# Kernel optimization log

Hardware: AMD Instinct MI355X
Metric: run time of the kernel (lower is better)

The kernel has to match this reference:

```python
import jax, jax.numpy as jnp
import numpy as np

K = 16  # hardcoded in the original forward
B, N, D = 4, 8192, 3


def _compute_normals_pca(x, k):
    """x: [B, N, 3] point cloud -> [B, N, 3] unit normals (smallest-eigvec of local covariance)."""
    sq = jnp.sum(x * x, axis=-1)  # [B, N]
    # squared pairwise distances [B, N, N]
    d2 = sq[:, :, None] + sq[:, None, :] - 2.0 * jnp.einsum('bnd,bmd->bnm', x, x)
    _, idx = jax.lax.top_k(-d2, k)  # k nearest (includes self), [B, N, k]
    # gather neighbor coordinates: [B, N, k, 3]
    nbrs = jax.vmap(lambda pts, i: pts[i])(x, idx)
    cen = nbrs - jnp.mean(nbrs, axis=2, keepdims=True)  # center per neighborhood
    cov = jnp.einsum('bnki,bnkj->bnij', cen, cen) / k   # [B, N, 3, 3]
    # eigh returns ascending eigenvalues; normal = eigvec of smallest eigenvalue (unit norm)
    evecs = jnp.linalg.eigh(cov)[1]
    return evecs[..., 0]  # [B, N, 3]


def setup_inputs() -> dict:
    key = jax.random.key(0)
    k1, k2 = jax.random.split(key)
    pred = jax.random.normal(k1, (B, N, D), dtype=jnp.float32)
    gt = jax.random.normal(k2, (B, N, D), dtype=jnp.float32)
    return {"pred": pred, "gt": gt}


def reference(pred, gt):
    n_pred = _compute_normals_pca(pred, K)
    n_gt = _compute_normals_pca(gt, K)
    return 1.0 - jnp.mean(jnp.sum(n_pred * n_gt, axis=-1))
```

## Files before the change

### kernel.cpp

```cpp
#include <hip/hip_runtime.h>
#include <math.h>


#define NPTS 8192
#define NB   4
#define QPW  4


__device__ __forceinline__ float slapy2f(float x, float y){
#pragma clang fp contract(off)
  float xa = fabsf(x), ya = fabsf(y);
  float w = fmaxf(xa, ya), z = fminf(xa, ya);
  if (z == 0.f) return w;
  float t = z / w;
  return w * sqrtf(1.f + t*t);
}

__device__ __forceinline__ void slartgf(float f, float g, float& c, float& s, float& r){
#pragma clang fp contract(off)
  const float safmin = 1.17549435e-38f;
  const float safmax = 8.50705917e37f;
  const float rtmin  = 1.08420217e-19f;
  const float rtmax  = 6.52318604e18f;
  if (g == 0.f){ c = 1.f; s = 0.f; r = f; }
  else if (f == 0.f){ c = 0.f; s = copysignf(1.f, g); r = fabsf(g); }
  else {
    float f1 = fabsf(f), g1 = fabsf(g);
    if (f1 > rtmin && f1 < rtmax && g1 > rtmin && g1 < rtmax){
      float d = sqrtf(f*f + g*g);
      c = f1 / d;
      r = copysignf(d, f);
      s = g / r;
    } else {
      float u = fminf(safmax, fmaxf(safmin, fmaxf(f1, g1)));
      float fs = f/u, gs = g/u;
      float d = sqrtf(fs*fs + gs*gs);
      c = fabsf(fs)/d;
      r = copysignf(d, f);
      r = r*u;
      s = g/r;
    }
  }
}

__device__ __forceinline__ void slaev2f(float a, float b, float cc,
                                        float& rt1, float& rt2, float& cs1, float& sn1){
#pragma clang fp contract(off)
  float sm  = a + cc;
  float df  = a - cc;
  float adf = fabsf(df);
  float tb  = b + b;
  float ab  = fabsf(tb);
  float acmx, acmn;
  if (fabsf(a) > fabsf(cc)){ acmx = a; acmn = cc; } else { acmx = cc; acmn = a; }
  float rt;
  if (adf > ab){ float t = ab/adf; rt = adf*sqrtf(1.f + t*t); }
  else if (adf < ab){ float t = adf/ab; rt = ab*sqrtf(1.f + t*t); }
  else rt = ab*sqrtf(2.f);
  int sgn1;
  if (sm < 0.f){ rt1 = 0.5f*(sm - rt); sgn1 = -1; rt2 = (acmx/rt1)*acmn - (b/rt1)*b; }
  else if (sm > 0.f){ rt1 = 0.5f*(sm + rt); sgn1 = 1; rt2 = (acmx/rt1)*acmn - (b/rt1)*b; }
  else { rt1 = 0.5f*rt; rt2 = -0.5f*rt; sgn1 = 1; }
  int sgn2; float cs;
  if (df >= 0.f){ cs = df + rt; sgn2 = 1; } else { cs = df - rt; sgn2 = -1; }
  float acs = fabsf(cs);
  if (acs > ab){ float ct = -tb/cs; sn1 = 1.f/sqrtf(1.f + ct*ct); cs1 = ct*sn1; }
  else {
    if (ab == 0.f){ cs1 = 1.f; sn1 = 0.f; }
    else { float tn = -cs/tb; cs1 = 1.f/sqrtf(1.f + tn*tn); sn1 = tn*cs1; }
  }
  if (sgn1 == sgn2){ float tn = cs1; cs1 = -sn1; sn1 = tn; }
}

__device__ __forceinline__ void rot2(float z[3][3], int ja, float c, float s){
#pragma clang fp contract(off)
  #pragma unroll
  for (int i = 0; i < 3; ++i){
    float t1 = z[i][ja+1];
    float t0 = z[i][ja];
    z[i][ja+1] = c*t1 - s*t0;
    z[i][ja]   = s*t1 + c*t0;
  }
}

__device__ __noinline__ void ssteqr3(float* d, float* e, float z[3][3]){
#pragma clang fp contract(off)
  const float eps    = 5.96046448e-08f;
  const float eps2   = 3.55271368e-15f;
  const float safmin = 1.17549435e-38f;
  const float ssfmax = 3.07445735e+18f;
  const float ssfmin = 3.05175781e-05f;
  const int n = 3;
  float cw[2], sw[2];
  int nmaxit, jtot, l1, l, lsv, lend, lendsv, m, iscale, i, j, ii, k;
  float anorm, p, g, r, c, s, f, b, rt1, rt2, tst, mul;

  for (i = 0; i < 3; ++i) for (j = 0; j < 3; ++j) z[i][j] = (i == j) ? 1.f : 0.f;
  nmaxit = n*30; jtot = 0; l1 = 1; m = 0; iscale = 0; anorm = 0.f;
  lsv = 1; lendsv = 1; lend = 1; l = 1;

L10:
  if (l1 > n) goto L160;
  if (l1 > 1) e[l1-2] = 0.f;
  if (l1 <= n-1){
    for (m = l1; m <= n-1; ++m){
      tst = fabsf(e[m-1]);
      if (tst == 0.f) goto L30;
      if (tst <= (sqrtf(fabsf(d[m-1]))*sqrtf(fabsf(d[m])))*eps){ e[m-1] = 0.f; goto L30; }
    }
  }
  m = n;
L30:
  l = l1; lsv = l; lend = m; lendsv = lend; l1 = m + 1;
  if (lend == l) goto L10;
  anorm = 0.f;
  for (i = l; i <= lend; ++i)   anorm = fmaxf(anorm, fabsf(d[i-1]));
  for (i = l; i <= lend-1; ++i) anorm = fmaxf(anorm, fabsf(e[i-1]));
  iscale = 0;
  if (anorm == 0.f) goto L10;
  if (anorm > ssfmax){
    iscale = 1; mul = ssfmax/anorm;
    for (i = l; i <= lend; ++i)   d[i-1] *= mul;
    for (i = l; i <= lend-1; ++i) e[i-1] *= mul;
  } else if (anorm < ssfmin){
    iscale = 2; mul = ssfmin/anorm;
    for (i = l; i <= lend; ++i)   d[i-1] *= mul;
    for (i = l; i <= lend-1; ++i) e[i-1] *= mul;
  }
  if (fabsf(d[lend-1]) < fabsf(d[l-1])){ lend = lsv; l = lendsv; }

  if (lend > l){
L40:
    if (l != lend){
      for (m = l; m <= lend-1; ++m){
        tst = fabsf(e[m-1]); tst = tst*tst;
        if (tst <= (eps2*fabsf(d[m-1]))*fabsf(d[m]) + safmin) goto L60;
      }
    }
    m = lend;
L60:
    if (m < lend) e[m-1] = 0.f;
    p = d[l-1];
    if (m == l) goto L80;
    if (m == l+1){
      slaev2f(d[l-1], e[l-1], d[l], rt1, rt2, c, s);
      rot2(z, l-1, c, s);
      d[l-1] = rt1; d[l] = rt2; e[l-1] = 0.f;
      l += 2;
      if (l <= lend) goto L40;
      goto L140;
    }
    if (jtot == nmaxit) goto L140;
    jtot++;
    g = (d[l] - p)/(2.f*e[l-1]);
    r = slapy2f(g, 1.f);
    g = d[m-1] - p + (e[l-1]/(g + copysignf(r, g)));
    s = 1.f; c = 1.f; p = 0.f;
    for (i = m-1; i >= l; --i){
      f = s*e[i-1];
      b = c*e[i-1];
      slartgf(g, f, c, s, r);
      if (i != m-1) e[i] = r;
      g = d[i] - p;
      r = (d[i-1] - g)*s + 2.f*c*b;
      p = s*r;
      d[i] = g + p;
      g = c*r - b;
      cw[i-l] = c; sw[i-l] = -s;
    }
    for (j = m-l; j >= 1; --j) rot2(z, l+j-2, cw[j-1], sw[j-1]);
    d[l-1] = d[l-1] - p;
    e[l-1] = g;
    goto L40;
L80:
    d[l-1] = p;
    l += 1;
    if (l <= lend) goto L40;
    goto L140;
  } else {
L90:
    if (l != lend){
      for (m = l; m >= lend+1; --m){
        tst = fabsf(e[m-2]); tst = tst*tst;
        if (tst <= (eps2*fabsf(d[m-1]))*fabsf(d[m-2]) + safmin) goto L110;
      }
    }
    m = lend;
L110:
    if (m > lend) e[m-2] = 0.f;
    p = d[l-1];
    if (m == l) goto L130;
    if (m == l-1){
      slaev2f(d[l-2], e[l-2], d[l-1], rt1, rt2, c, s);
      rot2(z, l-2, c, s);
      d[l-2] = rt1; d[l-1] = rt2; e[l-2] = 0.f;
      l -= 2;
      if (l >= lend) goto L90;
      goto L140;
    }
    if (jtot == nmaxit) goto L140;
    jtot++;
    g = (d[l-2] - p)/(2.f*e[l-2]);
    r = slapy2f(g, 1.f);
    g = d[m-1] - p + (e[l-2]/(g + copysignf(r, g)));
    s = 1.f; c = 1.f; p = 0.f;
    for (i = m; i <= l-1; ++i){
      f = s*e[i-1];
      b = c*e[i-1];
      slartgf(g, f, c, s, r);
      if (i != m) e[i-2] = r;
      g = d[i-1] - p;
      r = (d[i] - g)*s + 2.f*c*b;
      p = s*r;
      d[i-1] = g + p;
      g = c*r - b;
      cw[i-m] = c; sw[i-m] = s;
    }
    for (j = 1; j <= l-m; ++j) rot2(z, m+j-2, cw[j-1], sw[j-1]);
    d[l-1] = d[l-1] - p;
    e[l-2] = g;
    goto L90;
L130:
    d[l-1] = p;
    l -= 1;
    if (l >= lend) goto L90;
    goto L140;
  }
L140:
  if (iscale == 1){
    mul = anorm/ssfmax;
    for (i = lsv; i <= lendsv; ++i)   d[i-1] *= mul;
    for (i = lsv; i <= lendsv-1; ++i) e[i-1] *= mul;
  } else if (iscale == 2){
    mul = anorm/ssfmin;
    for (i = lsv; i <= lendsv; ++i)   d[i-1] *= mul;
    for (i = lsv; i <= lendsv-1; ++i) e[i-1] *= mul;
  }
  if (jtot < nmaxit) goto L10;
  return;
L160:
  for (ii = 2; ii <= n; ++ii){
    i = ii - 1; k = i; p = d[i-1];
    for (j = ii; j <= n; ++j){
      if (d[j-1] < p){ k = j; p = d[j-1]; }
    }
    if (k != i){
      d[k-1] = d[i-1]; d[i-1] = p;
      for (j = 0; j < 3; ++j){ float t = z[j][i-1]; z[j][i-1] = z[j][k-1]; z[j][k-1] = t; }
    }
  }
}

__device__ __noinline__ void eigh3_normal(float a11, float a21, float a31,
                                          float a22, float a32, float a33,
                                          float* out3){
#pragma clang fp contract(off)
  float d[3], e[2], z[3][3];
  float tau1 = 0.f, v2 = 0.f;
  float alpha = a21;
  float xnorm = fabsf(a31);
  if (xnorm == 0.f){
    e[0] = alpha;
    tau1 = 0.f;
  } else {
    float beta = -copysignf(slapy2f(alpha, xnorm), alpha);
    tau1 = (beta - alpha)/beta;
    v2 = a31*(1.f/(alpha - beta));
    float x1 = tau1*a22 + tau1*(a32*v2);
    float x2 = tau1*a32 + (tau1*v2)*a33;
    float al = -0.5f*tau1*(x1 + x2*v2);
    float w1 = x1 + al;
    float w2 = x2 + al*v2;
    a22 = a22 - w1 - w1;
    a32 = a32 - v2*w1 - w2;
    a33 = a33 - v2*w2 - w2*v2;
    e[0] = beta;
  }
  e[1] = a32;
  d[0] = a11; d[1] = a22; d[2] = a33;
  ssteqr3(d, e, z);
  if (tau1 != 0.f){
    #pragma unroll
    for (int jj = 0; jj < 3; ++jj){
      float wj  = z[1][jj] + v2*z[2][jj];
      float tmp = tau1*wj;
      z[1][jj] = z[1][jj] - tmp;
      z[2][jj] = z[2][jj] - v2*tmp;
    }
  }
  out3[0] = z[0][0]; out3[1] = z[1][0]; out3[2] = z[2][0];
}


__device__ __forceinline__ float sq3f(float x, float y, float z){
#pragma clang fp contract(off)
  return x*x + y*y + z*z;
}

__device__ __forceinline__ float d2f(float qs, float qx, float qy, float qz, float4 c){
#pragma clang fp contract(off)
  float dot = qx*c.x + qy*c.y + qz*c.z;
  return (qs + c.w) - 2.f*dot;
}


__global__ __launch_bounds__(256) void pack_kernel(const float* __restrict__ pred,
                                                   const float* __restrict__ gt,
                                                   float4* __restrict__ packed){
#pragma clang fp contract(off)
  int i = blockIdx.x*256 + threadIdx.x;
  int cloud = i >> 13;
  int p = i & 8191;
  const float* base = ((cloud >> 2) ? gt : pred) + (size_t)(cloud & 3)*(NPTS*3);
  float x = base[p*3+0], y = base[p*3+1], z = base[p*3+2];
  packed[i] = make_float4(x, y, z, sq3f(x, y, z));
}

__global__ __launch_bounds__(256) void select_kernel(const float4* __restrict__ packed,
                                                     unsigned short* __restrict__ topk){
#pragma clang fp contract(off)
  const int tid  = threadIdx.x;
  const int lane = tid & 63;
  const int g    = blockIdx.x*4 + (tid >> 6);
  const int qbase = g*QPW;
  const int pc   = qbase >> 13;
  const float4* __restrict__ cp = packed + (size_t)pc*NPTS;
  const int q0 = qbase & 8191;

  float4 qv[QPW];
  #pragma unroll
  for (int k = 0; k < QPW; ++k) qv[k] = cp[q0 + k];

  float thrA[QPW];
  #pragma unroll
  for (int k = 0; k < QPW; ++k)
    thrA[k] = fminf(0.0599f * __expf(qv[k].w * 0.33333334f), 0.8f);

  float bd[QPW]; int bi[QPW]; float t16[QPW]; int tI[QPW];
  bool done[QPW];
  #pragma unroll
  for (int k = 0; k < QPW; ++k) done[k] = false;

#define EV_INSERT(K, ddv, iv) {                                               \
    unsigned long long m = __ballot((ddv) <= thrA[K]);                        \
    while (m){                                                                \
      int s = __ffsll(m) - 1;                                                 \
      m &= m - 1;                                                             \
      float dds = __shfl((ddv), s);                                           \
      int idxs = (iv) + s;                                                    \
      if ((dds < t16[K]) || (dds == t16[K] && idxs < tI[K])){                 \
        bool less = (bd[K] < dds) || (bd[K] == dds && bi[K] < idxs);          \
        unsigned long long lm = __ballot(less) & 0xFFFFull;                   \
        int pos = __popcll(lm);                                               \
        float bup = __shfl_up(bd[K], 1);                                      \
        int   iup = __shfl_up(bi[K], 1);                                      \
        bool tn = (lane == pos);                                              \
        bool tu = (lane > pos) && (lane < 16);                                \
        bd[K] = tn ? dds  : (tu ? bup : bd[K]);                               \
        bi[K] = tn ? idxs : (tu ? iup : bi[K]);                               \
        t16[K] = __shfl(bd[K], 15);                                           \
        tI[K]  = __shfl(bi[K], 15);                                           \
      }                                                                       \
    }                                                                         \
  }

  #pragma unroll
  for (int k = 0; k < QPW; ++k){
    bd[k] = 3.0e38f; bi[k] = 0x7fffffff; t16[k] = 3.0e38f; tI[k] = 0x7fffffff;
  }
  for (int it = 0; it < NPTS/64; ++it){
    const int b0 = it*64;
    float4 cd = cp[b0 + lane];
    #pragma unroll
    for (int k = 0; k < QPW; ++k){
      float dd = d2f(qv[k].w, qv[k].x, qv[k].y, qv[k].z, cd);
      EV_INSERT(k, dd, b0)
    }
  }
  {
    bool anyUndone = false;
    #pragma unroll
    for (int k = 0; k < QPW; ++k){
      if (t16[k] < 3.0e38f) done[k] = true;
      else { thrA[k] = thrA[k]*2.5f + 1e-3f; anyUndone = true; }
    }
    for (int round = 1; round < 7 && anyUndone; ++round){
      #pragma unroll
      for (int k = 0; k < QPW; ++k) if (!done[k]){
        bd[k] = 3.0e38f; bi[k] = 0x7fffffff; t16[k] = 3.0e38f; tI[k] = 0x7fffffff;
      }
      for (int it = 0; it < NPTS/64; ++it){
        const int b0 = it*64;
        float4 cd = cp[b0 + lane];
        #pragma unroll
        for (int k = 0; k < QPW; ++k){
          if (done[k]) continue;
          float dd = d2f(qv[k].w, qv[k].x, qv[k].y, qv[k].z, cd);
          EV_INSERT(k, dd, b0)
        }
      }
      anyUndone = false;
      #pragma unroll
      for (int k = 0; k < QPW; ++k) if (!done[k]){
        if (t16[k] < 3.0e38f) done[k] = true;
        else { thrA[k] = thrA[k]*2.5f + 1e-3f; anyUndone = true; }
      }
    }
  }
#undef EV_INSERT

  if (lane < 16){
    #pragma unroll
    for (int k = 0; k < QPW; ++k)
      topk[(size_t)(qbase + k)*16 + lane] = (unsigned short)bi[k];
  }
}

__global__ __launch_bounds__(256) void normal_kernel(const float4* __restrict__ packed,
                                                     const unsigned short* __restrict__ topk,
                                                     float* __restrict__ normals){
#pragma clang fp contract(off)
  const int gq = blockIdx.x*256 + threadIdx.x;
  const int pc = gq >> 13;
  const float4* __restrict__ cp = packed + (size_t)pc*NPTS;
  const unsigned short* __restrict__ tk = topk + (size_t)gq*16;

  float gxx[16], gyy[16], gzz[16];
  #pragma unroll
  for (int r = 0; r < 16; ++r){
    float4 p = cp[tk[r]];
    gxx[r] = p.x; gyy[r] = p.y; gzz[r] = p.z;
  }
  float mx = 0.f, my = 0.f, mz = 0.f;
  #pragma unroll
  for (int r = 0; r < 16; ++r){ mx += gxx[r]; my += gyy[r]; mz += gzz[r]; }
  mx *= 0.0625f; my *= 0.0625f; mz *= 0.0625f;

  float c00=0.f, c10=0.f, c20=0.f, c11=0.f, c21=0.f, c22=0.f;
  #pragma unroll
  for (int r = 0; r < 16; ++r){
    float cx = gxx[r]-mx, cy = gyy[r]-my, cz = gzz[r]-mz;
    c00 += cx*cx; c10 += cy*cx; c20 += cz*cx;
    c11 += cy*cy; c21 += cz*cy; c22 += cz*cz;
  }
  c00 *= 0.0625f; c10 *= 0.0625f; c20 *= 0.0625f;
  c11 *= 0.0625f; c21 *= 0.0625f; c22 *= 0.0625f;

  float nrm[3];
  eigh3_normal(c00, c10, c20, c11, c21, c22, nrm);

  float* o = normals + (size_t)gq*3;
  o[0] = nrm[0]; o[1] = nrm[1]; o[2] = nrm[2];
}


__global__ __launch_bounds__(256) void loss_partial(const float* __restrict__ normals,
                                                    float* __restrict__ partials){
  __shared__ float red[256];
  const float4* a4 = (const float4*)normals;
  const float4* g4 = (const float4*)(normals + (size_t)NB*NPTS*3);
  float acc = 0.f;
  for (int i = blockIdx.x*256 + threadIdx.x; i < 24576; i += 64*256){
    float4 a = a4[i], g = g4[i];
    acc += a.x*g.x + a.y*g.y + a.z*g.z + a.w*g.w;
  }
  red[threadIdx.x] = acc;
  __syncthreads();
  for (int sft = 128; sft > 0; sft >>= 1){
    if (threadIdx.x < sft) red[threadIdx.x] += red[threadIdx.x + sft];
    __syncthreads();
  }
  if (threadIdx.x == 0) partials[blockIdx.x] = red[0];
}

__global__ void loss_final(const float* __restrict__ partials,
                           float* __restrict__ out){
  float v = partials[threadIdx.x];
  #pragma unroll
  for (int s = 32; s > 0; s >>= 1) v += __shfl_down(v, s, 64);
  if (threadIdx.x == 0) out[0] = 1.f - v*(1.f/32768.f);
}

extern "C" void kernel_launch(void* const* d_in, const int* in_sizes, int n_in,
                              void* d_out, int out_size, void* d_ws, size_t ws_size,
                              hipStream_t stream) {
  const float* pred = (const float*)d_in[0];
  const float* gt   = (const float*)d_in[1];
  float*          normals  = (float*)d_ws;
  float*          partials = normals + (size_t)2*NB*NPTS*3;
  float4*         packed   = (float4*)(partials + 64);
  unsigned short* topk     = (unsigned short*)(packed + (size_t)8*NPTS);
  pack_kernel  <<<256,  256, 0, stream>>>(pred, gt, packed);
  select_kernel<<<4096, 256, 0, stream>>>(packed, topk);
  normal_kernel<<<256,  256, 0, stream>>>(packed, topk, normals);
  loss_partial <<<64,   256, 0, stream>>>(normals, partials);
  loss_final   <<<1,     64, 0, stream>>>(partials, (float*)d_out);
}
```

Measured before the change: 381.9 us.

## Bucket-sort points by x and prune kNN search to nearby x-slab windows

Points are binned by x coordinate into 256 buckets using a histogram, prefix scan and scatter, so each cloud is stored sorted by x. The select kernel then scans outward from each query's position in 64-point chunks and stops once bucket edges lie beyond the current search radius, instead of scanning all 8192 candidates. This cuts distance evaluations and ballot work per query. In exchange it adds three small kernels plus a memset and uses atomic-ordered scatter, and tie-breaking now uses a composite original index.

```diff
diff --git a/kernel.cpp b/kernel.cpp
--- a/kernel.cpp
+++ b/kernel.cpp
@@ -303,20 +303,62 @@
   return (qs + c.w) - 2.f*dot;
 }
 
-
-__global__ __launch_bounds__(256) void pack_kernel(const float* __restrict__ pred,
+__device__ __forceinline__ int bucket_of(float x){
+#pragma clang fp contract(off)
+  return (int)fminf(fmaxf((x + 4.0f)*32.0f, 0.0f), 255.0f);
+}
+
+
+__global__ __launch_bounds__(256) void hist_kernel(const float* __restrict__ pred,
                                                    const float* __restrict__ gt,
-                                                   float4* __restrict__ packed){
+                                                   int* __restrict__ hist){
+  int i = blockIdx.x*256 + threadIdx.x;
+  int cloud = i >> 13;
+  int p = i & 8191;
+  const float* base = ((cloud >> 2) ? gt : pred) + (size_t)(cloud & 3)*(NPTS*3);
+  float x = base[p*3+0];
+  atomicAdd(&hist[cloud*256 + bucket_of(x)], 1);
+}
+
+__global__ void prefix_kernel(const int* __restrict__ hist, int* __restrict__ bstart){
+  __shared__ int buf[256];
+  const int t = threadIdx.x;
+  for (int c = 0; c < 8; ++c){
+    buf[t] = hist[c*256 + t];
+    __syncthreads();
+    for (int off = 1; off < 256; off <<= 1){
+      int u = (t >= off) ? buf[t - off] : 0;
+      __syncthreads();
+      buf[t] += u;
+      __syncthreads();
+    }
+    if (t == 0) bstart[c*257] = 0;
+    bstart[c*257 + t + 1] = buf[t];
+    __syncthreads();
+  }
+}
+
+__global__ __launch_bounds__(256) void scatter_kernel(const float* __restrict__ pred,
+                                                      const float* __restrict__ gt,
+                                                      const int* __restrict__ bstart,
+                                                      int* __restrict__ bfill,
+                                                      float4* __restrict__ bpts,
+                                                      unsigned int* __restrict__ binfo){
 #pragma clang fp contract(off)
   int i = blockIdx.x*256 + threadIdx.x;
   int cloud = i >> 13;
   int p = i & 8191;
   const float* base = ((cloud >> 2) ? gt : pred) + (size_t)(cloud & 3)*(NPTS*3);
   float x = base[p*3+0], y = base[p*3+1], z = base[p*3+2];
-  packed[i] = make_float4(x, y, z, sq3f(x, y, z));
-}
-
-__global__ __launch_bounds__(256) void select_kernel(const float4* __restrict__ packed,
+  int b = bucket_of(x);
+  int pos = bstart[cloud*257 + b] + atomicAdd(&bfill[cloud*256 + b], 1);
+  bpts [(size_t)cloud*NPTS + pos] = make_float4(x, y, z, sq3f(x, y, z));
+  binfo[(size_t)cloud*NPTS + pos] = ((unsigned int)p << 8) | (unsigned int)b;
+}
+
+
+__global__ __launch_bounds__(256) void select_kernel(const float4* __restrict__ bpts,
+                                                     const unsigned int* __restrict__ binfo,
                                                      unsigned short* __restrict__ topk){
 #pragma clang fp contract(off)
   const int tid  = threadIdx.x;
@@ -324,111 +366,131 @@
   const int g    = blockIdx.x*4 + (tid >> 6);
   const int qbase = g*QPW;
   const int pc   = qbase >> 13;
-  const float4* __restrict__ cp = packed + (size_t)pc*NPTS;
+  const float4*       __restrict__ bp = bpts  + (size_t)pc*NPTS;
+  const unsigned int* __restrict__ bf = binfo + (size_t)pc*NPTS;
   const int q0 = qbase & 8191;
 
   float4 qv[QPW];
   #pragma unroll
-  for (int k = 0; k < QPW; ++k) qv[k] = cp[q0 + k];
+  for (int k = 0; k < QPW; ++k) qv[k] = bp[q0 + k];
 
   float thrA[QPW];
   #pragma unroll
   for (int k = 0; k < QPW; ++k)
     thrA[k] = fminf(0.0599f * __expf(qv[k].w * 0.33333334f), 0.8f);
 
-  float bd[QPW]; int bi[QPW]; float t16[QPW]; int tI[QPW];
-  bool done[QPW];
+  float bd[QPW]; int bi[QPW]; float t16[QPW]; int tI[QPW]; bool done[QPW];
   #pragma unroll
   for (int k = 0; k < QPW; ++k) done[k] = false;
 
-#define EV_INSERT(K, ddv, iv) {                                               \
-    unsigned long long m = __ballot((ddv) <= thrA[K]);                        \
+  const int pR0 = q0 & ~63;
+
+#define EV_INSERT(K, ddv, civv, passv) {                                      \
+    unsigned long long m = __ballot(passv);                                   \
     while (m){                                                                \
       int s = __ffsll(m) - 1;                                                 \
       m &= m - 1;                                                             \
       float dds = __shfl((ddv), s);                                           \
-      int idxs = (iv) + s;                                                    \
-      if ((dds < t16[K]) || (dds == t16[K] && idxs < tI[K])){                 \
-        bool less = (bd[K] < dds) || (bd[K] == dds && bi[K] < idxs);          \
+      int cis = __shfl((civv), s);                                            \
+      if ((dds < t16[K]) || (dds == t16[K] && cis < tI[K])){                  \
+        bool less = (bd[K] < dds) || (bd[K] == dds && bi[K] < cis);           \
         unsigned long long lm = __ballot(less) & 0xFFFFull;                   \
         int pos = __popcll(lm);                                               \
         float bup = __shfl_up(bd[K], 1);                                      \
         int   iup = __shfl_up(bi[K], 1);                                      \
         bool tn = (lane == pos);                                              \
         bool tu = (lane > pos) && (lane < 16);                                \
-        bd[K] = tn ? dds  : (tu ? bup : bd[K]);                               \
-        bi[K] = tn ? idxs : (tu ? iup : bi[K]);                               \
+        bd[K] = tn ? dds : (tu ? bup : bd[K]);                                \
+        bi[K] = tn ? cis : (tu ? iup : bi[K]);                                \
         t16[K] = __shfl(bd[K], 15);                                           \
         tI[K]  = __shfl(bi[K], 15);                                           \
       }                                                                       \
     }                                                                         \
   }
 
-  #pragma unroll
-  for (int k = 0; k < QPW; ++k){
-    bd[k] = 3.0e38f; bi[k] = 0x7fffffff; t16[k] = 3.0e38f; tI[k] = 0x7fffffff;
-  }
-  for (int it = 0; it < NPTS/64; ++it){
-    const int b0 = it*64;
-    float4 cd = cp[b0 + lane];
+#define WIN_BOUNDS() {                                                        \
+    xmax = -3.0e38f; xmin = 3.0e38f;                                          \
+    _Pragma("unroll")                                                         \
+    for (int k = 0; k < QPW; ++k) if (!done[k]){                              \
+      float rr = sqrtf(fminf(thrA[k], t16[k])) + 1.0e-2f;                     \
+      xmax = fmaxf(xmax, qv[k].x + rr);                                       \
+      xmin = fminf(xmin, qv[k].x - rr);                                       \
+    }                                                                         \
+  }
+
+#define PROCESS_CHUNK(CS) {                                                   \
+    int pos = (CS) + lane;                                                    \
+    bool vmask = (pos >= 0) && (pos < NPTS);                                  \
+    int cpos = vmask ? pos : 0;                                               \
+    float4 cd = bp[cpos];                                                     \
+    unsigned int bnf = bf[cpos];                                              \
+    int civ = (int)(((bnf >> 8) << 13) | (unsigned int)cpos);                 \
+    _Pragma("unroll")                                                         \
+    for (int k = 0; k < QPW; ++k){                                            \
+      float dd = d2f(qv[k].w, qv[k].x, qv[k].y, qv[k].z, cd);                 \
+      bool pass = vmask && (!done[k]) && (dd <= fminf(thrA[k], t16[k]));      \
+      EV_INSERT(k, dd, civ, pass)                                             \
+    }                                                                         \
+  }
+
+  for (int round = 0; round < 7; ++round){
+    #pragma unroll
+    for (int k = 0; k < QPW; ++k) if (!done[k]){
+      bd[k] = 3.0e38f; bi[k] = 0x7fffffff; t16[k] = 3.0e38f; tI[k] = 0x7fffffff;
+    }
+    float xmax, xmin;
+    int pR = pR0;
+    while (pR < NPTS){
+      int jR = (int)(bf[pR] & 255u);
+      WIN_BOUNDS();
+      float eLo = (jR == 0) ? -3.0e38f : ((float)jR * 0.03125f - 4.0f);
+      if (eLo > xmax) break;
+      PROCESS_CHUNK(pR);
+      pR += 64;
+    }
+    int pL = pR0;
+    while (pL > 0){
+      int jL = (int)(bf[pL - 1] & 255u);
+      WIN_BOUNDS();
+      float eHi = (jL == 255) ? 3.0e38f : ((float)(jL + 1) * 0.03125f - 4.0f);
+      if (eHi < xmin) break;
+      PROCESS_CHUNK(pL - 64);
+      pL -= 64;
+    }
+    bool anyUn = false;
+    #pragma unroll
+    for (int k = 0; k < QPW; ++k) if (!done[k]){
+      if (t16[k] < 2.9e38f) done[k] = true;
+      else { anyUn = true; thrA[k] = (round >= 5) ? 1.0e30f : thrA[k]*2.5f + 1.0e-3f; }
+    }
+    if (!anyUn) break;
+  }
+#undef PROCESS_CHUNK
+#undef WIN_BOUNDS
+#undef EV_INSERT
+
+  if (lane < 16){
     #pragma unroll
     for (int k = 0; k < QPW; ++k){
-      float dd = d2f(qv[k].w, qv[k].x, qv[k].y, qv[k].z, cd);
-      EV_INSERT(k, dd, b0)
-    }
-  }
-  {
-    bool anyUndone = false;
-    #pragma unroll
-    for (int k = 0; k < QPW; ++k){
-      if (t16[k] < 3.0e38f) done[k] = true;
-      else { thrA[k] = thrA[k]*2.5f + 1e-3f; anyUndone = true; }
-    }
-    for (int round = 1; round < 7 && anyUndone; ++round){
-      #pragma unroll
-      for (int k = 0; k < QPW; ++k) if (!done[k]){
-        bd[k] = 3.0e38f; bi[k] = 0x7fffffff; t16[k] = 3.0e38f; tI[k] = 0x7fffffff;
-      }
-      for (int it = 0; it < NPTS/64; ++it){
-        const int b0 = it*64;
-        float4 cd = cp[b0 + lane];
-        #pragma unroll
-        for (int k = 0; k < QPW; ++k){
-          if (done[k]) continue;
-          float dd = d2f(qv[k].w, qv[k].x, qv[k].y, qv[k].z, cd);
-          EV_INSERT(k, dd, b0)
-        }
-      }
-      anyUndone = false;
-      #pragma unroll
-      for (int k = 0; k < QPW; ++k) if (!done[k]){
-        if (t16[k] < 3.0e38f) done[k] = true;
-        else { thrA[k] = thrA[k]*2.5f + 1e-3f; anyUndone = true; }
-      }
-    }
-  }
-#undef EV_INSERT
-
-  if (lane < 16){
-    #pragma unroll
-    for (int k = 0; k < QPW; ++k)
-      topk[(size_t)(qbase + k)*16 + lane] = (unsigned short)bi[k];
-  }
-}
-
-__global__ __launch_bounds__(256) void normal_kernel(const float4* __restrict__ packed,
+      int oq = (int)(bf[q0 + k] >> 8);
+      topk[((size_t)pc*NPTS + oq)*16 + lane] = (unsigned short)(bi[k] & 8191);
+    }
+  }
+}
+
+__global__ __launch_bounds__(256) void normal_kernel(const float4* __restrict__ bpts,
                                                      const unsigned short* __restrict__ topk,
                                                      float* __restrict__ normals){
 #pragma clang fp contract(off)
   const int gq = blockIdx.x*256 + threadIdx.x;
   const int pc = gq >> 13;
-  const float4* __restrict__ cp = packed + (size_t)pc*NPTS;
+  const float4* __restrict__ bp = bpts + (size_t)pc*NPTS;
   const unsigned short* __restrict__ tk = topk + (size_t)gq*16;
 
   float gxx[16], gyy[16], gzz[16];
   #pragma unroll
   for (int r = 0; r < 16; ++r){
-    float4 p = cp[tk[r]];
+    float4 p = bp[tk[r]];
     gxx[r] = p.x; gyy[r] = p.y; gzz[r] = p.z;
   }
   float mx = 0.f, my = 0.f, mz = 0.f;
@@ -486,13 +548,22 @@
                               hipStream_t stream) {
   const float* pred = (const float*)d_in[0];
   const float* gt   = (const float*)d_in[1];
-  float*          normals  = (float*)d_ws;
-  float*          partials = normals + (size_t)2*NB*NPTS*3;
-  float4*         packed   = (float4*)(partials + 64);
-  unsigned short* topk     = (unsigned short*)(packed + (size_t)8*NPTS);
-  pack_kernel  <<<256,  256, 0, stream>>>(pred, gt, packed);
-  select_kernel<<<4096, 256, 0, stream>>>(packed, topk);
-  normal_kernel<<<256,  256, 0, stream>>>(packed, topk, normals);
-  loss_partial <<<64,   256, 0, stream>>>(normals, partials);
-  loss_final   <<<1,     64, 0, stream>>>(partials, (float*)d_out);
-}
+  char* w = (char*)d_ws;
+  float*          normals  = (float*)(w);
+  float*          partials = (float*)(w + 786432);
+  int*            hist     = (int*)(w + 786688);
+  int*            bfill    = (int*)(w + 794880);
+  int*            bstart   = (int*)(w + 803072);
+  float4*         bpts     = (float4*)(w + 811296);
+  unsigned int*   binfo    = (unsigned int*)(w + 1859872);
+  unsigned short* topk     = (unsigned short*)(w + 2122016);
+
+  hipMemsetAsync(w + 786688, 0, 16384, stream);
+  hist_kernel   <<<256,  256, 0, stream>>>(pred, gt, hist);
+  prefix_kernel <<<1,    256, 0, stream>>>(hist, bstart);
+  scatter_kernel<<<256,  256, 0, stream>>>(pred, gt, bstart, bfill, bpts, binfo);
+  select_kernel <<<4096, 256, 0, stream>>>(bpts, binfo, topk);
+  normal_kernel <<<256,  256, 0, stream>>>(bpts, topk, normals);
+  loss_partial  <<<64,   256, 0, stream>>>(normals, partials);
+  loss_final    <<<1,     64, 0, stream>>>(partials, (float*)d_out);
+}
```

Result: slower. 505.3 us (+32.3%).
